# Kernel optimization log

Measured on AMD Instinct MI355X. Metric: run time of the kernel, lower is better.

Reference implementation:

```python
import jax, jax.numpy as jnp
import numpy as np

T, K, E, H, I = 1024, 2, 8, 2048, 1024


def setup_inputs() -> dict:
    key = jax.random.key(0)
    k1, k2, k3, k4 = jax.random.split(key, 4)
    hidden_states = jax.random.normal(k1, (T, H), dtype=jnp.float32)
    selected_experts = jax.random.randint(k2, (T, K), 0, E, dtype=jnp.int32)
    # glorot-ish scale for the batched expert kernels
    gu_scale = (2.0 / (H + 2 * I)) ** 0.5
    dn_scale = (2.0 / (I + H)) ** 0.5
    gate_up_proj = jax.random.normal(k3, (E, 2 * I, H), dtype=jnp.float32) * gu_scale
    down_proj = jax.random.normal(k4, (E, H, I), dtype=jnp.float32) * dn_scale
    return {
        "hidden_states": hidden_states,
        "selected_experts": selected_experts,
        "gate_up_proj": gate_up_proj,
        "down_proj": down_proj,
    }


def reference(hidden_states, selected_experts, gate_up_proj, down_proj):
    # Mathematically identical to the original per-token weight gather
    # (ops.take + 'th,temh->tem'), but expressed as dense all-expert GEMMs
    # followed by an output gather, avoiding the T*k*2I*H weight blowup.
    # gate_up_all: (T, E, 2I)
    gate_up_all = jnp.einsum("th,emh->tem", hidden_states, gate_up_proj)
    gate, up = jnp.split(gate_up_all, 2, axis=-1)
    intermediate = jax.nn.silu(gate) * up                # (T, E, I)
    out_all = jnp.einsum("tem,ehm->teh", intermediate, down_proj)  # (T, E, H)
    # select the top-k experts' outputs per token -> (T, K, H)
    return jnp.take_along_axis(out_all, selected_experts[..., None].astype(jnp.int32), axis=1)
```

## Files before the change

### kernel.cpp

```cpp
#include <hip/hip_runtime.h>
#include <hip/hip_bf16.h>

#define T_TOK 1024
#define KSEL  2
#define NEXP  8
#define HDIM  2048
#define IDIM  1024
#define TK    2048

#define BR 72

typedef float  f32x4  __attribute__((ext_vector_type(4)));
typedef __bf16 bf16x8 __attribute__((ext_vector_type(8)));
typedef __bf16 bf16x2 __attribute__((ext_vector_type(2)));

__device__ __forceinline__ unsigned short f2bf(float f) {
    union { float f; unsigned u; } v; v.f = f;
    unsigned r = (v.u >> 16) & 1u;
    return (unsigned short)((v.u + 0x7fffu + r) >> 16);
}

__device__ __forceinline__ unsigned pk2bf(float lo, float hi) {
#if __has_builtin(__builtin_amdgcn_cvt_pk_bf16_f32)
    bf16x2 v = __builtin_amdgcn_cvt_pk_bf16_f32(lo, hi);
    union { bf16x2 v; unsigned u; } c; c.v = v;
    return c.u;
#else
    return (unsigned)f2bf(lo) | ((unsigned)f2bf(hi) << 16);
#endif
}

__global__ __launch_bounds__(256) void prep(
    const float* __restrict__ hidden, const int* __restrict__ sel,
    unsigned short* __restrict__ hid_bf, int* __restrict__ meta,
    int* __restrict__ pairs)
{
    const int t = blockIdx.x * 256 + threadIdx.x;
    {
        const float* s = hidden + (size_t)t * 8;
        float4 v0 = *(const float4*)s;
        float4 v1 = *(const float4*)(s + 4);
        uint4 o;
        o.x = pk2bf(v0.x, v0.y); o.y = pk2bf(v0.z, v0.w);
        o.z = pk2bf(v1.x, v1.y); o.w = pk2bf(v1.z, v1.w);
        *(uint4*)(hid_bf + (size_t)t * 8) = o;
    }
    if (blockIdx.x == 0) {
        __shared__ int lcnt[NEXP], lstart[NEXP], lfill[NEXP];
        const int tid = threadIdx.x;
        if (tid < NEXP) { lcnt[tid] = 0; lfill[tid] = 0; }
        __syncthreads();
        for (int i = tid; i < TK; i += 256) atomicAdd(&lcnt[sel[i]], 1);
        __syncthreads();
        if (tid == 0) {
            int s2 = 0;
            for (int e2 = 0; e2 < NEXP; ++e2) { lstart[e2] = s2; s2 += lcnt[e2]; }
        }
        __syncthreads();
        for (int i = tid; i < TK; i += 256) {
            int e2 = sel[i];
            pairs[lstart[e2] + atomicAdd(&lfill[e2], 1)] = i;
        }
        if (tid < NEXP) { meta[tid] = lcnt[tid]; meta[NEXP + tid] = lstart[tid]; }
    }
}

__global__ __launch_bounds__(256, 2) void gemm1_gateup(
    const unsigned short* __restrict__ hid_bf, const float* __restrict__ gup,
    const int* __restrict__ meta, const int* __restrict__ pairs,
    unsigned short* __restrict__ inter)
{
    __shared__ __align__(16) unsigned short Bs[3][64 * BR];

    const int bx = blockIdx.x;
    const int e = bx & 7, nt = (bx >> 3) & 31, mt = bx >> 8;
    const int cnt = meta[e];
    const int m0 = mt * 192;
    if (m0 >= cnt) return;
    const int seg  = meta[8 + e];
    const int rows = cnt - m0;
    const int n0   = nt * 32;

    const int tid  = threadIdx.x;
    const int lane = tid & 63, w = tid >> 6;
    const int quad = lane >> 4, l16 = lane & 15;

    const int brow = tid >> 2, bkc = (tid & 3) * 16;
    const int grow = (brow < 32) ? (n0 + brow) : (IDIM + n0 + (brow - 32));
    const float* __restrict__ bp =
        gup + (size_t)e * (2 * IDIM * HDIM) + (size_t)grow * HDIM + bkc;
    const int bofs = brow * BR + bkc;

    const unsigned short* ap[3];
    #pragma unroll
    for (int i = 0; i < 3; ++i) {
        int mr  = m0 + w * 48 + i * 16 + l16;
        int idx = seg + min(mr, cnt - 1);
        ap[i] = hid_bf + (size_t)(pairs[idx] >> 1) * HDIM + quad * 8;
    }

    f32x4 accg[3][2], accu[3][2];
    const f32x4 zero = {0.f, 0.f, 0.f, 0.f};
    #pragma unroll
    for (int i = 0; i < 3; ++i)
        #pragma unroll
        for (int j = 0; j < 2; ++j) { accg[i][j] = zero; accu[i][j] = zero; }

    float4 Br0[4], Br1[4];
    bf16x8 afA[3][2], afB[3][2];

    auto loadB = [&](float4 (&br)[4], int s) {
        const float* p = bp + s * 64;
        #pragma unroll
        for (int c = 0; c < 4; ++c) br[c] = *(const float4*)(p + c * 4);
    };
    auto storeB = [&](const float4 (&br)[4], int buf) {
        uint4 o0, o1;
        o0.x = pk2bf(br[0].x, br[0].y); o0.y = pk2bf(br[0].z, br[0].w);
        o0.z = pk2bf(br[1].x, br[1].y); o0.w = pk2bf(br[1].z, br[1].w);
        o1.x = pk2bf(br[2].x, br[2].y); o1.y = pk2bf(br[2].z, br[2].w);
        o1.z = pk2bf(br[3].x, br[3].y); o1.w = pk2bf(br[3].z, br[3].w);
        *(uint4*)&Bs[buf][bofs]     = o0;
        *(uint4*)&Bs[buf][bofs + 8] = o1;
    };
    auto loadA = [&](bf16x8 (&af)[3][2], int s) {
        #pragma unroll
        for (int i = 0; i < 3; ++i)
            #pragma unroll
            for (int kk = 0; kk < 2; ++kk)
                af[i][kk] = *(const bf16x8*)(ap[i] + s * 64 + kk * 32);
    };
    auto compute = [&](const bf16x8 (&af)[3][2], int buf) {
        #pragma unroll
        for (int kk = 0; kk < 2; ++kk) {
            const int ko = kk * 32 + quad * 8;
            bf16x8 bg[2], bu[2];
            #pragma unroll
            for (int j = 0; j < 2; ++j) {
                bg[j] = *(const bf16x8*)&Bs[buf][(j * 16 + l16) * BR + ko];
                bu[j] = *(const bf16x8*)&Bs[buf][(32 + j * 16 + l16) * BR + ko];
            }
            #pragma unroll
            for (int i = 0; i < 3; ++i)
                #pragma unroll
                for (int j = 0; j < 2; ++j) {
                    accg[i][j] = __builtin_amdgcn_mfma_f32_16x16x32_bf16(af[i][kk], bg[j], accg[i][j], 0, 0, 0);
                    accu[i][j] = __builtin_amdgcn_mfma_f32_16x16x32_bf16(af[i][kk], bu[j], accu[i][j], 0, 0, 0);
                }
        }
    };

    const int NK = HDIM / 64;
    loadB(Br0, 0);
    loadA(afA, 0);
    storeB(Br0, 0);
    loadB(Br0, 1);
    loadB(Br1, 2);
    __syncthreads();

    for (int s = 0; s < NK; s += 2) {
        storeB(Br0, (s + 1) % 3);
        if (s + 3 < NK) loadB(Br0, s + 3);
        loadA(afB, s + 1);
        compute(afA, s % 3);
        __syncthreads();
        if (s + 2 < NK) storeB(Br1, (s + 2) % 3);
        if (s + 4 < NK) loadB(Br1, s + 4);
        if (s + 2 < NK) loadA(afA, s + 2);
        compute(afB, (s + 1) % 3);
        __syncthreads();
    }

    #pragma unroll
    for (int i = 0; i < 3; ++i) {
        #pragma unroll
        for (int r = 0; r < 4; ++r) {
            int mrow = w * 48 + i * 16 + quad * 4 + r;
            if (mrow < rows && mrow < 192) {
                size_t orow = (size_t)(seg + m0 + mrow) * IDIM;
                #pragma unroll
                for (int j = 0; j < 2; ++j) {
                    float g = accg[i][j][r], u = accu[i][j][r];
                    float sv = g * (1.f / (1.f + __expf(-g)));
                    inter[orow + n0 + j * 16 + l16] = f2bf(sv * u);
                }
            }
        }
    }
}

__global__ __launch_bounds__(256, 2) void gemm2_down(
    const unsigned short* __restrict__ inter, const float* __restrict__ down,
    const int* __restrict__ meta, const int* __restrict__ pairs,
    float* __restrict__ out)
{
    __shared__ __align__(16) unsigned short Bs[3][64 * BR];

    const int bx = blockIdx.x;
    const int e = bx & 7, nt = (bx >> 3) & 31, mt = bx >> 8;
    const int cnt = meta[e];
    const int m0 = mt * 192;
    if (m0 >= cnt) return;
    const int seg  = meta[8 + e];
    const int rows = cnt - m0;
    const int n0   = nt * 64;

    const int tid  = threadIdx.x;
    const int lane = tid & 63, w = tid >> 6;
    const int quad = lane >> 4, l16 = lane & 15;

    const int brow = tid >> 2, bkc = (tid & 3) * 16;
    const float* __restrict__ bp =
        down + (size_t)e * (HDIM * IDIM) + (size_t)(n0 + brow) * IDIM + bkc;
    const int bofs = brow * BR + bkc;

    const unsigned short* ap[3];
    #pragma unroll
    for (int i = 0; i < 3; ++i) {
        int mr  = m0 + w * 48 + i * 16 + l16;
        int idx = seg + min(mr, cnt - 1);
        ap[i] = inter + (size_t)idx * IDIM + quad * 8;
    }

    f32x4 acc[3][4];
    const f32x4 zero = {0.f, 0.f, 0.f, 0.f};
    #pragma unroll
    for (int i = 0; i < 3; ++i)
        #pragma unroll
        for (int j = 0; j < 4; ++j) acc[i][j] = zero;

    float4 Br0[4], Br1[4];
    bf16x8 afA[3][2], afB[3][2];

    auto loadB = [&](float4 (&br)[4], int s) {
        const float* p = bp + s * 64;
        #pragma unroll
        for (int c = 0; c < 4; ++c) br[c] = *(const float4*)(p + c * 4);
    };
    auto storeB = [&](const float4 (&br)[4], int buf) {
        uint4 o0, o1;
        o0.x = pk2bf(br[0].x, br[0].y); o0.y = pk2bf(br[0].z, br[0].w);
        o0.z = pk2bf(br[1].x, br[1].y); o0.w = pk2bf(br[1].z, br[1].w);
        o1.x = pk2bf(br[2].x, br[2].y); o1.y = pk2bf(br[2].z, br[2].w);
        o1.z = pk2bf(br[3].x, br[3].y); o1.w = pk2bf(br[3].z, br[3].w);
        *(uint4*)&Bs[buf][bofs]     = o0;
        *(uint4*)&Bs[buf][bofs + 8] = o1;
    };
    auto loadA = [&](bf16x8 (&af)[3][2], int s) {
        #pragma unroll
        for (int i = 0; i < 3; ++i)
            #pragma unroll
            for (int kk = 0; kk < 2; ++kk)
                af[i][kk] = *(const bf16x8*)(ap[i] + s * 64 + kk * 32);
    };
    auto compute = [&](const bf16x8 (&af)[3][2], int buf) {
        #pragma unroll
        for (int kk = 0; kk < 2; ++kk) {
            const int ko = kk * 32 + quad * 8;
            bf16x8 bf[4];
            #pragma unroll
            for (int j = 0; j < 4; ++j)
                bf[j] = *(const bf16x8*)&Bs[buf][(j * 16 + l16) * BR + ko];
            #pragma unroll
            for (int i = 0; i < 3; ++i)
                #pragma unroll
                for (int j = 0; j < 4; ++j)
                    acc[i][j] = __builtin_amdgcn_mfma_f32_16x16x32_bf16(af[i][kk], bf[j], acc[i][j], 0, 0, 0);
        }
    };

    const int NK = IDIM / 64;
    loadB(Br0, 0);
    loadA(afA, 0);
    storeB(Br0, 0);
    loadB(Br0, 1);
    loadB(Br1, 2);
    __syncthreads();

    for (int s = 0; s < NK; s += 2) {
        storeB(Br0, (s + 1) % 3);
        if (s + 3 < NK) loadB(Br0, s + 3);
        loadA(afB, s + 1);
        compute(afA, s % 3);
        __syncthreads();
        if (s + 2 < NK) storeB(Br1, (s + 2) % 3);
        if (s + 4 < NK) loadB(Br1, s + 4);
        if (s + 2 < NK) loadA(afA, s + 2);
        compute(afB, (s + 1) % 3);
        __syncthreads();
    }

    #pragma unroll
    for (int i = 0; i < 3; ++i) {
        #pragma unroll
        for (int r = 0; r < 4; ++r) {
            int mrow = w * 48 + i * 16 + quad * 4 + r;
            if (mrow < rows && mrow < 192) {
                int p = pairs[seg + m0 + mrow];
                size_t ob = (size_t)p * HDIM + n0 + l16;
                #pragma unroll
                for (int j = 0; j < 4; ++j)
                    out[ob + j * 16] = acc[i][j][r];
            }
        }
    }
}

extern "C" void kernel_launch(void* const* d_in, const int* in_sizes, int n_in,
                              void* d_out, int out_size, void* d_ws, size_t ws_size,
                              hipStream_t stream) {
    const float* hidden = (const float*)d_in[0];
    const int*   sel    = (const int*)  d_in[1];
    const float* gup    = (const float*)d_in[2];
    const float* down   = (const float*)d_in[3];
    float* out = (float*)d_out;

    char* ws = (char*)d_ws;
    int* meta  = (int*)ws;
    int* pairs = meta + 16;
    unsigned short* inter  = (unsigned short*)(ws + 16384);
    unsigned short* hid_bf = inter + (size_t)TK * IDIM;

    prep<<<T_TOK * HDIM / 8 / 256, 256, 0, stream>>>(hidden, sel, hid_bf, meta, pairs);
    gemm1_gateup<<<2 * 32 * 8, 256, 0, stream>>>(hid_bf, gup, meta, pairs, inter);
    gemm2_down  <<<2 * 32 * 8, 256, 0, stream>>>(inter, down, meta, pairs, out);
}
```

Before: 292.4 us.

## Interleave B-tile global loads across threads and reshape register pipeline

```diff
diff --git a/kernel.cpp b/kernel.cpp
--- a/kernel.cpp
+++ b/kernel.cpp
@@ -85,11 +85,15 @@
     const int lane = tid & 63, w = tid >> 6;
     const int quad = lane >> 4, l16 = lane & 15;
 
-    const int brow = tid >> 2, bkc = (tid & 3) * 16;
-    const int grow = (brow < 32) ? (n0 + brow) : (IDIM + n0 + (brow - 32));
-    const float* __restrict__ bp =
-        gup + (size_t)e * (2 * IDIM * HDIM) + (size_t)grow * HDIM + bkc;
-    const int bofs = brow * BR + bkc;
+    const float* bp[4]; int bofs[4];
+    #pragma unroll
+    for (int c = 0; c < 4; ++c) {
+        int id = tid + c * 256;
+        int brow = id >> 4, kc = id & 15;
+        int grow = (brow < 32) ? (n0 + brow) : (IDIM + n0 + (brow - 32));
+        bp[c]   = gup + (size_t)e * (2 * IDIM * HDIM) + (size_t)grow * HDIM + kc * 4;
+        bofs[c] = brow * BR + kc * 4;
+    }
 
     const unsigned short* ap[3];
     #pragma unroll
@@ -106,22 +110,23 @@
         #pragma unroll
         for (int j = 0; j < 2; ++j) { accg[i][j] = zero; accu[i][j] = zero; }
 
-    float4 Br0[4], Br1[4];
-    bf16x8 afA[3][2], afB[3][2];
-
-    auto loadB = [&](float4 (&br)[4], int s) {
-        const float* p = bp + s * 64;
-        #pragma unroll
-        for (int c = 0; c < 4; ++c) br[c] = *(const float4*)(p + c * 4);
-    };
-    auto storeB = [&](const float4 (&br)[4], int buf) {
-        uint4 o0, o1;
-        o0.x = pk2bf(br[0].x, br[0].y); o0.y = pk2bf(br[0].z, br[0].w);
-        o0.z = pk2bf(br[1].x, br[1].y); o0.w = pk2bf(br[1].z, br[1].w);
-        o1.x = pk2bf(br[2].x, br[2].y); o1.y = pk2bf(br[2].z, br[2].w);
-        o1.z = pk2bf(br[3].x, br[3].y); o1.w = pk2bf(br[3].z, br[3].w);
-        *(uint4*)&Bs[buf][bofs]     = o0;
-        *(uint4*)&Bs[buf][bofs + 8] = o1;
+    float4 X[4], Y[4];
+    bf16x8 afC[3][2], afN[3][2];
+
+    auto loadB = [&](float4 (&R)[4], int s) {
+        #pragma unroll
+        for (int c = 0; c < 4; ++c) R[c] = *(const float4*)(bp[c] + s * 64);
+    };
+    auto storeB = [&](const float4 (&R)[4], int buf) {
+        #pragma unroll
+        for (int c = 0; c < 4; ++c) {
+            ushort4 o;
+            o.x = (unsigned short)(pk2bf(R[c].x, R[c].y) & 0xffff);
+            o.y = (unsigned short)(pk2bf(R[c].x, R[c].y) >> 16);
+            o.z = (unsigned short)(pk2bf(R[c].z, R[c].w) & 0xffff);
+            o.w = (unsigned short)(pk2bf(R[c].z, R[c].w) >> 16);
+            *(ushort4*)&Bs[buf][bofs[c]] = o;
+        }
     };
     auto loadA = [&](bf16x8 (&af)[3][2], int s) {
         #pragma unroll
@@ -151,23 +156,21 @@
     };
 
     const int NK = HDIM / 64;
-    loadB(Br0, 0);
-    loadA(afA, 0);
-    storeB(Br0, 0);
-    loadB(Br0, 1);
-    loadB(Br1, 2);
+    loadB(X, 0);
+    loadB(Y, 1);
+    loadA(afC, 0);
+    storeB(X, 0);
     __syncthreads();
 
     for (int s = 0; s < NK; s += 2) {
-        storeB(Br0, (s + 1) % 3);
-        if (s + 3 < NK) loadB(Br0, s + 3);
-        loadA(afB, s + 1);
-        compute(afA, s % 3);
-        __syncthreads();
-        if (s + 2 < NK) storeB(Br1, (s + 2) % 3);
-        if (s + 4 < NK) loadB(Br1, s + 4);
-        if (s + 2 < NK) loadA(afA, s + 2);
-        compute(afB, (s + 1) % 3);
+        if (s + 2 < NK) loadB(X, s + 2);
+        loadA(afN, s + 1);
+        storeB(Y, (s + 1) % 3);
+        compute(afC, s % 3);
+        __syncthreads();
+        if (s + 3 < NK) loadB(Y, s + 3);
+        if (s + 2 < NK) { loadA(afC, s + 2); storeB(X, (s + 2) % 3); }
+        compute(afN, (s + 1) % 3);
         __syncthreads();
     }
 
@@ -209,10 +212,14 @@
     const int lane = tid & 63, w = tid >> 6;
     const int quad = lane >> 4, l16 = lane & 15;
 
-    const int brow = tid >> 2, bkc = (tid & 3) * 16;
-    const float* __restrict__ bp =
-        down + (size_t)e * (HDIM * IDIM) + (size_t)(n0 + brow) * IDIM + bkc;
-    const int bofs = brow * BR + bkc;
+    const float* bp[4]; int bofs[4];
+    #pragma unroll
+    for (int c = 0; c < 4; ++c) {
+        int id = tid + c * 256;
+        int brow = id >> 4, kc = id & 15;
+        bp[c]   = down + (size_t)e * (HDIM * IDIM) + (size_t)(n0 + brow) * IDIM + kc * 4;
+        bofs[c] = brow * BR + kc * 4;
+    }
 
     const unsigned short* ap[3];
     #pragma unroll
@@ -229,22 +236,23 @@
         #pragma unroll
         for (int j = 0; j < 4; ++j) acc[i][j] = zero;
 
-    float4 Br0[4], Br1[4];
-    bf16x8 afA[3][2], afB[3][2];
-
-    auto loadB = [&](float4 (&br)[4], int s) {
-        const float* p = bp + s * 64;
-        #pragma unroll
-        for (int c = 0; c < 4; ++c) br[c] = *(const float4*)(p + c * 4);
-    };
-    auto storeB = [&](const float4 (&br)[4], int buf) {
-        uint4 o0, o1;
-        o0.x = pk2bf(br[0].x, br[0].y); o0.y = pk2bf(br[0].z, br[0].w);
-        o0.z = pk2bf(br[1].x, br[1].y); o0.w = pk2bf(br[1].z, br[1].w);
-        o1.x = pk2bf(br[2].x, br[2].y); o1.y = pk2bf(br[2].z, br[2].w);
-        o1.z = pk2bf(br[3].x, br[3].y); o1.w = pk2bf(br[3].z, br[3].w);
-        *(uint4*)&Bs[buf][bofs]     = o0;
-        *(uint4*)&Bs[buf][bofs + 8] = o1;
+    float4 X[4], Y[4];
+    bf16x8 afC[3][2], afN[3][2];
+
+    auto loadB = [&](float4 (&R)[4], int s) {
+        #pragma unroll
+        for (int c = 0; c < 4; ++c) R[c] = *(const float4*)(bp[c] + s * 64);
+    };
+    auto storeB = [&](const float4 (&R)[4], int buf) {
+        #pragma unroll
+        for (int c = 0; c < 4; ++c) {
+            ushort4 o;
+            o.x = (unsigned short)(pk2bf(R[c].x, R[c].y) & 0xffff);
+            o.y = (unsigned short)(pk2bf(R[c].x, R[c].y) >> 16);
+            o.z = (unsigned short)(pk2bf(R[c].z, R[c].w) & 0xffff);
+            o.w = (unsigned short)(pk2bf(R[c].z, R[c].w) >> 16);
+            *(ushort4*)&Bs[buf][bofs[c]] = o;
+        }
     };
     auto loadA = [&](bf16x8 (&af)[3][2], int s) {
         #pragma unroll
@@ -270,23 +278,21 @@
     };
 
     const int NK = IDIM / 64;
-    loadB(Br0, 0);
-    loadA(afA, 0);
-    storeB(Br0, 0);
-    loadB(Br0, 1);
-    loadB(Br1, 2);
+    loadB(X, 0);
+    loadB(Y, 1);
+    loadA(afC, 0);
+    storeB(X, 0);
     __syncthreads();
 
     for (int s = 0; s < NK; s += 2) {
-        storeB(Br0, (s + 1) % 3);
-        if (s + 3 < NK) loadB(Br0, s + 3);
-        loadA(afB, s + 1);
-        compute(afA, s % 3);
-        __syncthreads();
-        if (s + 2 < NK) storeB(Br1, (s + 2) % 3);
-        if (s + 4 < NK) loadB(Br1, s + 4);
-        if (s + 2 < NK) loadA(afA, s + 2);
-        compute(afB, (s + 1) % 3);
+        if (s + 2 < NK) loadB(X, s + 2);
+        loadA(afN, s + 1);
+        storeB(Y, (s + 1) % 3);
+        compute(afC, s % 3);
+        __syncthreads();
+        if (s + 3 < NK) loadB(Y, s + 3);
+        if (s + 2 < NK) { loadA(afC, s + 2); storeB(X, (s + 2) % 3); }
+        compute(afN, (s + 1) % 3);
         __syncthreads();
     }
 
```

After: 289.8 us. About the same (-0.9%).
